# Optimization experiments

Hardware: AMD Instinct MI355X
Metric: run time of the kernel (lower is better)

The kernel has to match this reference:

```python
import jax, jax.numpy as jnp
import numpy as np

B, L, DIM, HEADS = 4, 1024, 512, 8
HD = DIM // HEADS
HID = max(64, DIM // 2)
WIN = 32
SPARSITY = 0.3
TEMP = 1.0
PAT_TAU = 0.5


def setup_inputs() -> dict:
    key = jax.random.key(0)
    ks = jax.random.split(key, 8)
    gn = lambda k, shape, sc: jax.random.normal(k, shape, jnp.float32) * sc
    return {
        "x": jax.random.normal(ks[0], (B, L, DIM), jnp.float32),
        "mask": jnp.ones((B, L), jnp.int32),
        "Wqkv": gn(ks[1], (3 * DIM, DIM), 0.02),
        "Wproj": gn(ks[2], (DIM, DIM), 0.02),
        "bproj": jnp.zeros((DIM,), jnp.float32),
        "Wsel1": gn(ks[3], (HID, DIM), 0.05),
        "bsel1": jnp.zeros((HID,), jnp.float32),
        "Wsel2": gn(ks[4], (3, HID), 0.05),
        "bsel2": jnp.zeros((3,), jnp.float32),
        "log_pattern_tau": jnp.asarray(np.log(PAT_TAU), jnp.float32),
        "sparse_w": gn(ks[5], (HEADS,), 0.2),
        "sparse_b": jnp.zeros((HEADS,), jnp.float32),
    }


def reference(x, mask, Wqkv, Wproj, bproj, Wsel1, bsel1, Wsel2, bsel2,
              log_pattern_tau, sparse_w, sparse_b):
    Bq, Lq, D = x.shape
    scale = HD ** -0.5
    qkv = (x @ Wqkv.T).reshape(Bq, Lq, 3, HEADS, HD)
    q = jnp.transpose(qkv[:, :, 0], (0, 2, 1, 3))  # (B,H,L,hd)
    k = jnp.transpose(qkv[:, :, 1], (0, 2, 1, 3))
    v = jnp.transpose(qkv[:, :, 2], (0, 2, 1, 3))
    scores = jnp.einsum('bhid,bhjd->bhij', q, k) * scale  # (B,H,L,L)

    # pattern selector on mean-pooled features (eval: no gumbel, no dropout)
    pooled = x.mean(axis=1)
    logits = jax.nn.relu(pooled @ Wsel1.T + bsel1) @ Wsel2.T + bsel2  # (B,3)
    tau = jnp.clip(jnp.exp(log_pattern_tau), 1e-4, 10.0)
    pw = jax.nn.softmax(logits / tau, axis=-1)  # (B,3)

    half = WIN // 2
    ii = jnp.arange(Lq)[:, None]
    jj = jnp.arange(Lq)[None, :]
    local = ((jj >= ii - half) & (jj <= ii + half)).astype(jnp.float32)

    # learned sparse top-k mask per head via kth-value threshold
    kk = max(1, int(Lq * (1.0 - SPARSITY)))
    s = scores * sparse_w[None, :, None, None] + sparse_b[None, :, None, None]
    kth = jax.lax.top_k(s, kk)[0][..., -1:]
    smask = (s >= kth).astype(jnp.float32)  # (B,H,L,L)

    combined = (pw[:, 0, None, None, None] * local[None, None]
                + pw[:, 1, None, None, None]
                + pw[:, 2, None, None, None] * smask)
    neg = jnp.float32(-1e9)
    scores = jnp.where(combined > 0.05, scores, neg)
    scores = jnp.where(mask[:, None, None, :] == 0, neg, scores)

    # fallback: if a row is fully masked, unmask position 0
    all_masked = jnp.all(scores <= neg + 1e-6, axis=-1)  # (B,H,L)
    scores = scores.at[..., 0].set(jnp.where(all_masked, 0.0, scores[..., 0]))

    attn = jax.nn.softmax(scores / TEMP, axis=-1)
    out = jnp.einsum('bhij,bhjd->bhid', attn, v)
    out = jnp.transpose(out, (0, 2, 1, 3)).reshape(Bq, Lq, D)
    return out @ Wproj.T + bproj
```

## Files before the change

kernel.cpp:

```cpp
#include <hip/hip_runtime.h>
#include <math.h>

typedef __attribute__((ext_vector_type(8))) short short8;
typedef __attribute__((ext_vector_type(4))) float floatx4;

#define MFMA16(a, b, c) __builtin_amdgcn_mfma_f32_16x16x32_bf16(a, b, c, 0, 0, 0)


#define FRAG512(row, k) (((size_t)((row) >> 4)) * 8192 + (((k) >> 5) * 512) + \
                         ((((k) >> 3) & 3) * 128) + (((row) & 15) * 8) + ((k) & 7))
#define FRAGQK(row, e)  (((size_t)((row) >> 4)) * 1024 + (((e) >> 5) * 512) + \
                         ((((e) >> 3) & 3) * 128) + (((row) & 15) * 8) + ((e) & 7))
#define FRAGV(key, e)   (((size_t)((key) >> 7)) * 8192 + \
                         ((((e) >> 4) * 4 + (((key) & 127) >> 5)) * 512) + \
                         (((((key) & 31) >> 3) * 16 + ((e) & 15)) * 8) + ((key) & 7))

#define OFF_XB    ((size_t)0)
#define OFF_WQKV  ((size_t)4194304)
#define OFF_WPROJ ((size_t)5767168)
#define OFF_Q     ((size_t)6291456)
#define OFF_K     ((size_t)10485760)
#define OFF_VT    ((size_t)14680064)
#define OFF_AT    ((size_t)18874368)
#define OFF_PW    ((size_t)23068672)
#define OFF_PAR   ((size_t)23069696)

__device__ __forceinline__ unsigned short f2bf(float f) {
    unsigned u = __float_as_uint(f);
    return (unsigned short)((u + 0x7fffu + ((u >> 16) & 1u)) >> 16);
}
__device__ __forceinline__ float bf2f(unsigned short s) {
    return __uint_as_float((unsigned)s << 16);
}
__device__ __forceinline__ void gl16(const void* g, void* l) {
    __builtin_amdgcn_global_load_lds(
        (const __attribute__((address_space(1))) unsigned*)g,
        (__attribute__((address_space(3))) unsigned*)l, 16, 0, 0);
}

__device__ __forceinline__ void frag_cvt_tile(const float* __restrict__ src,
                                              unsigned short* __restrict__ dst,
                                              const int t, const float sc)
{
    const int ln = t & 15, quad = (t >> 4) & 3, kh = t >> 6;
    #pragma unroll
    for (int i = 0; i < 4; ++i) {
        const int kb = kh + i * 4;
        const float* s = src + (size_t)ln * 512 + kb * 32 + quad * 8;
        float4 f0 = *(const float4*)s;
        float4 f1 = *(const float4*)(s + 4);
        unsigned short o[8] = { f2bf(f0.x * sc), f2bf(f0.y * sc), f2bf(f0.z * sc), f2bf(f0.w * sc),
                                f2bf(f1.x * sc), f2bf(f1.y * sc), f2bf(f1.z * sc), f2bf(f1.w * sc) };
        unsigned short* d = dst + kb * 512 + (size_t)(t & 63) * 8;
        *(ushort4*)d       = make_ushort4(o[0], o[1], o[2], o[3]);
        *(ushort4*)(d + 4) = make_ushort4(o[4], o[5], o[6], o[7]);
    }
}

__global__ __launch_bounds__(256)
void cvt_all(const float* __restrict__ x, const float* __restrict__ wqkv,
             const float* __restrict__ wproj, unsigned short* __restrict__ xb,
             unsigned short* __restrict__ oq, unsigned short* __restrict__ op,
             float* __restrict__ partial)
{
    const int bid = blockIdx.x, t = threadIdx.x;
    if (bid < 256) {
        const int b = bid >> 6, lb = bid & 63;
        const size_t base = ((size_t)b * 1024 + lb * 16) * 512;
        float s0 = 0.f, s1 = 0.f;
        #pragma unroll 4
        for (int l = 0; l < 16; ++l) {
            s0 += x[base + (size_t)l * 512 + t];
            s1 += x[base + (size_t)l * 512 + t + 256];
        }
        partial[((size_t)b * 64 + lb) * 512 + t] = s0;
        partial[((size_t)b * 64 + lb) * 512 + t + 256] = s1;
    } else if (bid < 512) {
        const int rt = bid - 256;
        frag_cvt_tile(x + (size_t)rt * 16 * 512, xb + (size_t)rt * 8192, t, 1.f);
    } else {
        const int tile = bid - 512;
        if (tile < 96)
            frag_cvt_tile(wqkv + (size_t)tile * 16 * 512, oq + (size_t)tile * 8192, t, 1.f);
        else
            frag_cvt_tile(wproj + (size_t)(tile - 96) * 16 * 512,
                          op + (size_t)(tile - 96) * 8192, t, 1.f);
    }
}

__global__ __launch_bounds__(256)
void selector_kernel(const float* __restrict__ partial,
                     const float* __restrict__ W1, const float* __restrict__ b1,
                     const float* __restrict__ W2, const float* __restrict__ b2,
                     const float* __restrict__ ltau, float* __restrict__ pwout)
{
    __shared__ float pooled[512];
    __shared__ float h1[256];
    __shared__ float lg[3];
    const int b = blockIdx.x, t = threadIdx.x;
    float s0 = 0.f, s1 = 0.f;
    for (int p = 0; p < 64; ++p) {
        s0 += partial[((size_t)b * 64 + p) * 512 + t];
        s1 += partial[((size_t)b * 64 + p) * 512 + t + 256];
    }
    pooled[t]       = s0 * (1.f / 1024.f);
    pooled[t + 256] = s1 * (1.f / 1024.f);
    __syncthreads();
    float acc = b1[t];
    const float* w1 = W1 + (size_t)t * 512;
    for (int d = 0; d < 512; d += 4) {
        float4 w4 = *(const float4*)(w1 + d);
        acc += w4.x * pooled[d] + w4.y * pooled[d + 1] + w4.z * pooled[d + 2] + w4.w * pooled[d + 3];
    }
    h1[t] = fmaxf(acc, 0.f);
    __syncthreads();
    if (t < 3) {
        float a = b2[t];
        const float* w2 = W2 + t * 256;
        for (int i = 0; i < 256; ++i) a += w2[i] * h1[i];
        float tauv = fminf(fmaxf(expf(ltau[0]), 1e-4f), 10.f);
        lg[t] = a / tauv;
    }
    __syncthreads();
    if (t == 0) {
        float m = fmaxf(lg[0], fmaxf(lg[1], lg[2]));
        float e0 = expf(lg[0] - m), e1 = expf(lg[1] - m), e2 = expf(lg[2] - m);
        float inv = 1.f / (e0 + e1 + e2);
        pwout[b * 3 + 0] = e0 * inv;
        pwout[b * 3 + 1] = e1 * inv;
        pwout[b * 3 + 2] = e2 * inv;
    }
}

__global__ __launch_bounds__(256)
void gemm_qkv(const unsigned short* __restrict__ xb, const unsigned short* __restrict__ wb,
              unsigned short* __restrict__ qo, unsigned short* __restrict__ ko,
              unsigned short* __restrict__ vo)
{
    __shared__ __align__(16) char smem[36864];
    unsigned short* As = (unsigned short*)smem;
    unsigned short* Bs = (unsigned short*)(smem + 8192);

    const int t = threadIdx.x;
    const int w = t >> 6, l64 = t & 63;
    const int ln = l64 & 15, quad = l64 >> 4;
    const int bx = blockIdx.x, by = blockIdx.y;
    const int m0 = by << 7, n0 = bx << 7;
    const int mw = (w & 1) << 6, nw = (w >> 1) << 6;

    floatx4 acc[4][4];
    #pragma unroll
    for (int i = 0; i < 4; ++i)
        #pragma unroll
        for (int j = 0; j < 4; ++j) acc[i][j] = (floatx4){0.f, 0.f, 0.f, 0.f};

    for (int s = 0; s < 16; ++s) {
        const int kb = s;
        #pragma unroll
        for (int ii = 0; ii < 2; ++ii) {
            const int bi = w * 2 + ii;
            gl16(xb + ((size_t)((m0 >> 4) + bi)) * 8192 + kb * 512 + l64 * 8,
                 (char*)As + bi * 1024);
            gl16(wb + ((size_t)((n0 >> 4) + bi)) * 8192 + kb * 512 + l64 * 8,
                 (char*)Bs + bi * 1024);
        }
        __syncthreads();
        short8 af[4], bf[4];
        #pragma unroll
        for (int i = 0; i < 4; ++i)
            af[i] = *(const short8*)((const char*)As + ((mw >> 4) + i) * 1024 + l64 * 16);
        #pragma unroll
        for (int j = 0; j < 4; ++j)
            bf[j] = *(const short8*)((const char*)Bs + ((nw >> 4) + j) * 1024 + l64 * 16);
        #pragma unroll
        for (int i = 0; i < 4; ++i)
            #pragma unroll
            for (int j = 0; j < 4; ++j)
                acc[i][j] = MFMA16(af[i], bf[j], acc[i][j]);
        __syncthreads();
    }

    unsigned short* tw = (unsigned short*)(smem + w * 9216);
    const int which = bx >> 2;
    const int hh = ((n0 + nw) >> 6) & 7;
    const int g = (by >> 3) * 8 + hh;
    const int lrow0 = (m0 & 1023) + mw;

    if (which == 2) {
        #pragma unroll
        for (int j = 0; j < 4; ++j)
            #pragma unroll
            for (int i = 0; i < 4; ++i)
                #pragma unroll
                for (int reg = 0; reg < 4; ++reg)
                    tw[(j * 16 + ln) * 72 + i * 16 + quad * 4 + reg] = f2bf(acc[i][j][reg]);
        const int chunk = lrow0 >> 7;
        const int ks0 = (lrow0 & 127) >> 5;
        unsigned short* dst = vo + (size_t)g * 65536 + (size_t)chunk * 8192;
        #pragma unroll
        for (int et = 0; et < 4; ++et)
            #pragma unroll
            for (int ksl = 0; ksl < 2; ++ksl) {
                const unsigned short* srcp = &tw[(et * 16 + ln) * 72 + ksl * 32 + quad * 8];
                *(short8*)(dst + (et * 4 + ks0 + ksl) * 512 + l64 * 8) = *(const short8*)srcp;
            }
    } else {
        const float sc = (which == 0) ? 0.125f : 1.f;
        #pragma unroll
        for (int j = 0; j < 4; ++j)
            #pragma unroll
            for (int i = 0; i < 4; ++i)
                #pragma unroll
                for (int reg = 0; reg < 4; ++reg)
                    tw[(i * 16 + quad * 4 + reg) * 72 + j * 16 + ln] = f2bf(acc[i][j][reg] * sc);
        unsigned short* dst = (which == 0 ? qo : ko) + (size_t)g * 65536;
        #pragma unroll
        for (int rt = 0; rt < 4; ++rt)
            #pragma unroll
            for (int eh = 0; eh < 2; ++eh) {
                const unsigned short* srcp = &tw[(rt * 16 + ln) * 72 + eh * 32 + quad * 8];
                *(short8*)(dst + ((size_t)((lrow0 >> 4) + rt)) * 1024 + eh * 512 + l64 * 8) =
                    *(const short8*)srcp;
            }
    }
}

__global__ __launch_bounds__(256)
void gemm_proj(const unsigned short* __restrict__ ab, const unsigned short* __restrict__ wb,
               const float* __restrict__ bias, float* __restrict__ out)
{
    __shared__ __align__(16) unsigned short As[8 * 512];
    __shared__ __align__(16) unsigned short Bs[4 * 512];
    const int t = threadIdx.x;
    const int w = t >> 6, l64 = t & 63;
    const int ln = l64 & 15, quad = l64 >> 4;
    const int n0 = blockIdx.x << 6;
    const int m0 = blockIdx.y << 7;
    const int mw = (w & 1) << 6, nw = (w >> 1) << 5;

    floatx4 acc[4][2];
    #pragma unroll
    for (int i = 0; i < 4; ++i)
        #pragma unroll
        for (int j = 0; j < 2; ++j) acc[i][j] = (floatx4){0.f, 0.f, 0.f, 0.f};

    for (int s = 0; s < 16; ++s) {
        #pragma unroll
        for (int ii = 0; ii < 2; ++ii) {
            const int bi = w * 2 + ii;
            gl16(ab + ((size_t)((m0 >> 4) + bi)) * 8192 + s * 512 + l64 * 8,
                 (char*)As + bi * 1024);
        }
        gl16(wb + ((size_t)((n0 >> 4) + w)) * 8192 + s * 512 + l64 * 8,
             (char*)Bs + w * 1024);
        __syncthreads();
        short8 af[4], bf[2];
        #pragma unroll
        for (int i = 0; i < 4; ++i)
            af[i] = *(const short8*)((const char*)As + ((mw >> 4) + i) * 1024 + l64 * 16);
        #pragma unroll
        for (int j = 0; j < 2; ++j)
            bf[j] = *(const short8*)((const char*)Bs + ((nw >> 4) + j) * 1024 + l64 * 16);
        #pragma unroll
        for (int i = 0; i < 4; ++i)
            #pragma unroll
            for (int j = 0; j < 2; ++j)
                acc[i][j] = MFMA16(af[i], bf[j], acc[i][j]);
        __syncthreads();
    }
    #pragma unroll
    for (int j = 0; j < 2; ++j) {
        const float bv = bias[n0 + nw + j * 16 + ln];
        #pragma unroll
        for (int i = 0; i < 4; ++i)
            #pragma unroll
            for (int reg = 0; reg < 4; ++reg)
                out[(size_t)(m0 + mw + i * 16 + quad * 4 + reg) * 512 + n0 + nw + j * 16 + ln] =
                    acc[i][j][reg] + bv;
    }
}

__global__ __launch_bounds__(256)
void attn_mfma(const unsigned short* __restrict__ qm, const unsigned short* __restrict__ km,
               const unsigned short* __restrict__ vm, const int* __restrict__ mask,
               const float* __restrict__ pw, const float* __restrict__ sw,
               const float* __restrict__ sb, unsigned short* __restrict__ aout)
{
    __shared__ int mk[1024];
    __shared__ float PO[4][16][68];
    __shared__ float msh[4][16], lsh[4][16];
    __shared__ unsigned kths[4][16];

    const int t = threadIdx.x;
    const int w = t >> 6, l64 = t & 63;
    const int ln = l64 & 15, quad = l64 >> 4;
    const int g = blockIdx.x & 31;
    const int rt = blockIdx.x >> 5;
    const int b = g >> 3, h = g & 7;
    const int i0 = rt * 16;

    const unsigned short* qg = qm + (size_t)g * 65536;
    const unsigned short* kg = km + (size_t)g * 65536;
    const unsigned short* vg = vm + (size_t)g * 65536;

    *(int4*)&mk[t * 4] = *(const int4*)(mask + b * 1024 + t * 4);

    const float pw0 = pw[b * 3 + 0], pw1 = pw[b * 3 + 1], pw2 = pw[b * 3 + 2];
    const bool a00 = pw1 > 0.05f;
    const bool a10 = (pw0 * 1.0f + pw1) > 0.05f;
    const bool a01 = (pw1 + pw2) > 0.05f;
    const bool a11 = ((pw0 * 1.0f + pw1) + pw2) > 0.05f;
    const bool need_sparse = (!a00 && a01) || (!a10 && a11);
    const bool flat_ok = (!need_sparse) && a00 && a10;
    const float w_h = sw[h], b_h = sb[h];
    __syncthreads();

    unsigned kth_r[4] = {0u, 0u, 0u, 0u};
    if (need_sparse) {
        unsigned* ub = (unsigned*)&PO[w][0][0];
        for (int r = 0; r < 16; ++r) {
            for (int c = 0; c < 16; ++c) {
                const int col = c * 64 + l64;
                float s = 0.f;
                for (int e = 0; e < 64; ++e)
                    s += bf2f(qg[FRAGQK(i0 + r, e)]) * bf2f(kg[FRAGQK(col, e)]);
                unsigned uu = __float_as_uint(s * w_h + b_h);
                ub[col] = (uu & 0x80000000u) ? ~uu : (uu | 0x80000000u);
            }
            unsigned u[16];
            #pragma unroll
            for (int c = 0; c < 16; ++c) u[c] = ub[l64 + c * 64];
            unsigned act = 0xFFFFu, p = 0u;
            int kk = 716;
            for (int bit = 31; bit >= 0; --bit) {
                unsigned ones = 0u;
                #pragma unroll
                for (int c = 0; c < 16; ++c)
                    if (((act >> c) & 1u) && ((u[c] >> bit) & 1u)) ones |= (1u << c);
                int c1 = __popc(ones);
                for (int off = 32; off; off >>= 1) c1 += __shfl_xor(c1, off);
                if (kk <= c1) { p |= (1u << bit); act &= ones; }
                else          { kk -= c1; act &= ~ones; }
            }
            if (l64 == 0) kths[w][r] = p;
        }
        #pragma unroll
        for (int reg = 0; reg < 4; ++reg) kth_r[reg] = kths[w][quad * 4 + reg];
    }

    const short8 aq0 = *(const short8*)(qg + ((size_t)(i0 >> 4)) * 1024 + l64 * 8);
    const short8 aq1 = *(const short8*)(qg + ((size_t)(i0 >> 4)) * 1024 + 512 + l64 * 8);

    float m_r[4] = {-3e38f, -3e38f, -3e38f, -3e38f};
    float l_r[4] = {0.f, 0.f, 0.f, 0.f};
    floatx4 accv[4];
    #pragma unroll
    for (int et = 0; et < 4; ++et) accv[et] = (floatx4){0.f, 0.f, 0.f, 0.f};
    unsigned short* Pw = (unsigned short*)&PO[w][0][0];

    #pragma unroll
    for (int cc = 0; cc < 2; ++cc) {
        const int j0 = (w * 2 + cc) << 7;
        const bool mall = __all((mk[j0 + l64] != 0) && (mk[j0 + 64 + l64] != 0));
        const bool fast = flat_ok && mall;

        const unsigned short* kbase = kg + ((size_t)(j0 >> 4)) * 1024 + l64 * 8;
        short8 kb0[8], kb1[8];
        #pragma unroll
        for (int nt = 0; nt < 8; ++nt) {
            kb0[nt] = *(const short8*)(kbase + nt * 1024);
            kb1[nt] = *(const short8*)(kbase + nt * 1024 + 512);
        }
        const unsigned short* vbase = vg + ((size_t)(j0 >> 7)) * 8192 + l64 * 8;
        short8 vb_cur[4], vb_nxt[4];
        #pragma unroll
        for (int ks = 0; ks < 4; ++ks)
            vb_cur[ks] = *(const short8*)(vbase + ks * 512);

        floatx4 sfr[8];
        #pragma unroll
        for (int nt = 0; nt < 8; ++nt) {
            floatx4 z = (floatx4){0.f, 0.f, 0.f, 0.f};
            z = MFMA16(aq0, kb0[nt], z);
            z = MFMA16(aq1, kb1[nt], z);
            sfr[nt] = z;
        }

        float rm[4] = {-3e38f, -3e38f, -3e38f, -3e38f};
        if (fast) {
            #pragma unroll
            for (int nt = 0; nt < 8; ++nt)
                #pragma unroll
                for (int reg = 0; reg < 4; ++reg) rm[reg] = fmaxf(rm[reg], sfr[nt][reg]);
        } else {
            #pragma unroll
            for (int nt = 0; nt < 8; ++nt) {
                const int j = j0 + nt * 16 + ln;
                const bool mk0 = (mk[j] == 0);
                #pragma unroll
                for (int reg = 0; reg < 4; ++reg) {
                    const int i = i0 + quad * 4 + reg;
                    const float s = sfr[nt][reg];
                    const bool loc = (j >= i - 16) && (j <= i + 16);
                    bool sm = false;
                    if (need_sparse) {
                        unsigned uu = __float_as_uint(s * w_h + b_h);
                        unsigned key = (uu & 0x80000000u) ? ~uu : (uu | 0x80000000u);
                        sm = key >= kth_r[reg];
                    }
                    bool allowed = loc ? (sm ? a11 : a10) : (sm ? a01 : a00);
                    if (mk0) allowed = false;
                    const float se = allowed ? s : -1e9f;
                    sfr[nt][reg] = se;
                    rm[reg] = fmaxf(rm[reg], se);
                }
            }
        }
        #pragma unroll
        for (int reg = 0; reg < 4; ++reg) {
            float v = rm[reg];
            v = fmaxf(v, __shfl_xor(v, 1));
            v = fmaxf(v, __shfl_xor(v, 2));
            v = fmaxf(v, __shfl_xor(v, 4));
            v = fmaxf(v, __shfl_xor(v, 8));
            rm[reg] = v;
        }
        float alpha[4], rs[4];
        #pragma unroll
        for (int reg = 0; reg < 4; ++reg) {
            const float mn = fmaxf(m_r[reg], rm[reg]);
            alpha[reg] = __expf(m_r[reg] - mn);
            m_r[reg] = mn;
            rs[reg] = 0.f;
        }
        #pragma unroll
        for (int nt = 0; nt < 8; ++nt)
            #pragma unroll
            for (int reg = 0; reg < 4; ++reg) {
                const float p = __expf(sfr[nt][reg] - m_r[reg]);
                rs[reg] += p;
                Pw[(quad * 4 + reg) * 136 + nt * 16 + ln] = f2bf(p);
            }
        #pragma unroll
        for (int reg = 0; reg < 4; ++reg) {
            float v = rs[reg];
            v += __shfl_xor(v, 1);
            v += __shfl_xor(v, 2);
            v += __shfl_xor(v, 4);
            v += __shfl_xor(v, 8);
            l_r[reg] = l_r[reg] * alpha[reg] + v;
        }
        short8 pa[4];
        #pragma unroll
        for (int ks = 0; ks < 4; ++ks)
            pa[ks] = *(const short8*)&Pw[ln * 136 + ks * 32 + quad * 8];
        #pragma unroll
        for (int et = 0; et < 4; ++et) {
            if (et < 3) {
                #pragma unroll
                for (int ks = 0; ks < 4; ++ks)
                    vb_nxt[ks] = *(const short8*)(vbase + ((et + 1) * 4 + ks) * 512);
            }
            floatx4 a = accv[et];
            a[0] *= alpha[0]; a[1] *= alpha[1]; a[2] *= alpha[2]; a[3] *= alpha[3];
            #pragma unroll
            for (int ks = 0; ks < 4; ++ks) a = MFMA16(pa[ks], vb_cur[ks], a);
            accv[et] = a;
            #pragma unroll
            for (int ks = 0; ks < 4; ++ks) vb_cur[ks] = vb_nxt[ks];
        }
    }

    #pragma unroll
    for (int et = 0; et < 4; ++et)
        #pragma unroll
        for (int reg = 0; reg < 4; ++reg)
            PO[w][quad * 4 + reg][et * 16 + ln] = accv[et][reg];
    if (ln == 0) {
        #pragma unroll
        for (int reg = 0; reg < 4; ++reg) {
            msh[w][quad * 4 + reg] = m_r[reg];
            lsh[w][quad * 4 + reg] = l_r[reg];
        }
    }
    __syncthreads();

    {
        const int r = t >> 4, cb = (t & 15) * 4;
        float M = fmaxf(fmaxf(msh[0][r], msh[1][r]), fmaxf(msh[2][r], msh[3][r]));
        float L = 0.f;
        float4 o = make_float4(0.f, 0.f, 0.f, 0.f);
        #pragma unroll
        for (int wv = 0; wv < 4; ++wv) {
            const float sc = __expf(msh[wv][r] - M);
            L += lsh[wv][r] * sc;
            float4 ov = *(const float4*)&PO[wv][r][cb];
            o.x += ov.x * sc; o.y += ov.y * sc; o.z += ov.z * sc; o.w += ov.w * sc;
        }
        ushort4 res;
        if (M <= -1e9f + 1e-6f) {
            res.x = vg[((cb + 0) >> 4) * 2048 + ((cb + 0) & 15) * 8];
            res.y = vg[((cb + 1) >> 4) * 2048 + ((cb + 1) & 15) * 8];
            res.z = vg[((cb + 2) >> 4) * 2048 + ((cb + 2) & 15) * 8];
            res.w = vg[((cb + 3) >> 4) * 2048 + ((cb + 3) & 15) * 8];
        } else {
            const float inv = 1.f / L;
            res.x = f2bf(o.x * inv); res.y = f2bf(o.y * inv);
            res.z = f2bf(o.z * inv); res.w = f2bf(o.w * inv);
        }
        const int row_g = b * 1024 + i0 + r;
        const int col = h * 64 + cb;
        *(ushort4*)&aout[FRAG512(row_g, col)] = res;
    }
}

extern "C" void kernel_launch(void* const* d_in, const int* in_sizes, int n_in,
                              void* d_out, int out_size, void* d_ws, size_t ws_size,
                              hipStream_t stream) {
    const float* x     = (const float*)d_in[0];
    const int*   mask  = (const int*)d_in[1];
    const float* Wqkv  = (const float*)d_in[2];
    const float* Wproj = (const float*)d_in[3];
    const float* bproj = (const float*)d_in[4];
    const float* Wsel1 = (const float*)d_in[5];
    const float* bsel1 = (const float*)d_in[6];
    const float* Wsel2 = (const float*)d_in[7];
    const float* bsel2 = (const float*)d_in[8];
    const float* ltau  = (const float*)d_in[9];
    const float* sw    = (const float*)d_in[10];
    const float* sb    = (const float*)d_in[11];
    char* ws = (char*)d_ws;
    unsigned short* xb     = (unsigned short*)(ws + OFF_XB);
    unsigned short* wqkvb  = (unsigned short*)(ws + OFF_WQKV);
    unsigned short* wprojb = (unsigned short*)(ws + OFF_WPROJ);
    unsigned short* q      = (unsigned short*)(ws + OFF_Q);
    unsigned short* k      = (unsigned short*)(ws + OFF_K);
    unsigned short* v      = (unsigned short*)(ws + OFF_VT);
    unsigned short* attnb  = (unsigned short*)(ws + OFF_AT);
    float* pw  = (float*)(ws + OFF_PW);
    float* par = (float*)(ws + OFF_PAR);
    float* out = (float*)d_out;
    (void)in_sizes; (void)n_in; (void)out_size; (void)ws_size;

    cvt_all<<<640, 256, 0, stream>>>(x, Wqkv, Wproj, xb, wqkvb, wprojb, par);
    selector_kernel<<<4, 256, 0, stream>>>(par, Wsel1, bsel1, Wsel2, bsel2, ltau, pw);
    gemm_qkv<<<dim3(12, 32), 256, 0, stream>>>(xb, wqkvb, q, k, v);
    attn_mfma<<<2048, 256, 0, stream>>>(q, k, v, mask, pw, sw, sb, attnb);
    gemm_proj<<<dim3(8, 32), 256, 0, stream>>>(attnb, wprojb, bproj, out);
}
```

Before: 163.8 us.

## Fuse selector into QKV GEMM and load MFMA fragments directly to registers

```diff
diff --git a/kernel.cpp b/kernel.cpp
--- a/kernel.cpp
+++ b/kernel.cpp
@@ -11,9 +11,6 @@
                          ((((k) >> 3) & 3) * 128) + (((row) & 15) * 8) + ((k) & 7))
 #define FRAGQK(row, e)  (((size_t)((row) >> 4)) * 1024 + (((e) >> 5) * 512) + \
                          ((((e) >> 3) & 3) * 128) + (((row) & 15) * 8) + ((e) & 7))
-#define FRAGV(key, e)   (((size_t)((key) >> 7)) * 8192 + \
-                         ((((e) >> 4) * 4 + (((key) & 127) >> 5)) * 512) + \
-                         (((((key) & 31) >> 3) * 16 + ((e) & 15)) * 8) + ((key) & 7))
 
 #define OFF_XB    ((size_t)0)
 #define OFF_WQKV  ((size_t)4194304)
@@ -31,11 +28,6 @@
 }
 __device__ __forceinline__ float bf2f(unsigned short s) {
     return __uint_as_float((unsigned)s << 16);
-}
-__device__ __forceinline__ void gl16(const void* g, void* l) {
-    __builtin_amdgcn_global_load_lds(
-        (const __attribute__((address_space(1))) unsigned*)g,
-        (__attribute__((address_space(3))) unsigned*)l, 16, 0, 0);
 }
 
 __device__ __forceinline__ void frag_cvt_tile(const float* __restrict__ src,
@@ -88,65 +80,70 @@
     }
 }
 
-__global__ __launch_bounds__(256)
-void selector_kernel(const float* __restrict__ partial,
-                     const float* __restrict__ W1, const float* __restrict__ b1,
-                     const float* __restrict__ W2, const float* __restrict__ b2,
-                     const float* __restrict__ ltau, float* __restrict__ pwout)
+__global__ __launch_bounds__(128)
+void gemm_qkv_sel(const unsigned short* __restrict__ xb, const unsigned short* __restrict__ wb,
+                  unsigned short* __restrict__ qo, unsigned short* __restrict__ ko,
+                  unsigned short* __restrict__ vo,
+                  const float* __restrict__ partial, const float* __restrict__ W1,
+                  const float* __restrict__ b1, const float* __restrict__ W2,
+                  const float* __restrict__ b2, const float* __restrict__ ltau,
+                  float* __restrict__ pwout)
 {
-    __shared__ float pooled[512];
-    __shared__ float h1[256];
-    __shared__ float lg[3];
-    const int b = blockIdx.x, t = threadIdx.x;
-    float s0 = 0.f, s1 = 0.f;
-    for (int p = 0; p < 64; ++p) {
-        s0 += partial[((size_t)b * 64 + p) * 512 + t];
-        s1 += partial[((size_t)b * 64 + p) * 512 + t + 256];
-    }
-    pooled[t]       = s0 * (1.f / 1024.f);
-    pooled[t + 256] = s1 * (1.f / 1024.f);
-    __syncthreads();
-    float acc = b1[t];
-    const float* w1 = W1 + (size_t)t * 512;
-    for (int d = 0; d < 512; d += 4) {
-        float4 w4 = *(const float4*)(w1 + d);
-        acc += w4.x * pooled[d] + w4.y * pooled[d + 1] + w4.z * pooled[d + 2] + w4.w * pooled[d + 3];
-    }
-    h1[t] = fmaxf(acc, 0.f);
-    __syncthreads();
-    if (t < 3) {
-        float a = b2[t];
-        const float* w2 = W2 + t * 256;
-        for (int i = 0; i < 256; ++i) a += w2[i] * h1[i];
-        float tauv = fminf(fmaxf(expf(ltau[0]), 1e-4f), 10.f);
-        lg[t] = a / tauv;
-    }
-    __syncthreads();
-    if (t == 0) {
-        float m = fmaxf(lg[0], fmaxf(lg[1], lg[2]));
-        float e0 = expf(lg[0] - m), e1 = expf(lg[1] - m), e2 = expf(lg[2] - m);
-        float inv = 1.f / (e0 + e1 + e2);
-        pwout[b * 3 + 0] = e0 * inv;
-        pwout[b * 3 + 1] = e1 * inv;
-        pwout[b * 3 + 2] = e2 * inv;
-    }
-}
-
-__global__ __launch_bounds__(256)
-void gemm_qkv(const unsigned short* __restrict__ xb, const unsigned short* __restrict__ wb,
-              unsigned short* __restrict__ qo, unsigned short* __restrict__ ko,
-              unsigned short* __restrict__ vo)
-{
-    __shared__ __align__(16) char smem[36864];
-    unsigned short* As = (unsigned short*)smem;
-    unsigned short* Bs = (unsigned short*)(smem + 8192);
-
+    __shared__ __align__(16) unsigned short tile[2][64 * 72];
+    const int bx = blockIdx.x, by = blockIdx.y;
     const int t = threadIdx.x;
+
+    if (by == 64) {
+        if (bx >= 4) return;
+        float* pooled = (float*)&tile[0][0];
+        float* h1 = pooled + 512;
+        float* lg = h1 + 256;
+        const int b = bx;
+        #pragma unroll
+        for (int c = 0; c < 4; ++c) {
+            const int col = t + c * 128;
+            float s = 0.f;
+            for (int p = 0; p < 64; ++p) s += partial[((size_t)b * 64 + p) * 512 + col];
+            pooled[col] = s * (1.f / 1024.f);
+        }
+        __syncthreads();
+        for (int r = t; r < 256; r += 128) {
+            float acc = b1[r];
+            const float* w1 = W1 + (size_t)r * 512;
+            for (int d = 0; d < 512; d += 4) {
+                float4 w4 = *(const float4*)(w1 + d);
+                acc += w4.x * pooled[d] + w4.y * pooled[d + 1] +
+                       w4.z * pooled[d + 2] + w4.w * pooled[d + 3];
+            }
+            h1[r] = fmaxf(acc, 0.f);
+        }
+        __syncthreads();
+        if (t < 3) {
+            float a = b2[t];
+            const float* w2 = W2 + t * 256;
+            for (int i = 0; i < 256; ++i) a += w2[i] * h1[i];
+            float tauv = fminf(fmaxf(expf(ltau[0]), 1e-4f), 10.f);
+            lg[t] = a / tauv;
+        }
+        __syncthreads();
+        if (t == 0) {
+            float m = fmaxf(lg[0], fmaxf(lg[1], lg[2]));
+            float e0 = expf(lg[0] - m), e1 = expf(lg[1] - m), e2 = expf(lg[2] - m);
+            float inv = 1.f / (e0 + e1 + e2);
+            pwout[b * 3 + 0] = e0 * inv;
+            pwout[b * 3 + 1] = e1 * inv;
+            pwout[b * 3 + 2] = e2 * inv;
+        }
+        return;
+    }
+
     const int w = t >> 6, l64 = t & 63;
     const int ln = l64 & 15, quad = l64 >> 4;
-    const int bx = blockIdx.x, by = blockIdx.y;
-    const int m0 = by << 7, n0 = bx << 7;
-    const int mw = (w & 1) << 6, nw = (w >> 1) << 6;
+    const int m0 = by << 6;
+    const int nb0 = (bx << 7) + (w << 6);
+
+    const unsigned short* Abase = xb + ((size_t)(m0 >> 4)) * 8192 + l64 * 8;
+    const unsigned short* Bbase = wb + ((size_t)(nb0 >> 4)) * 8192 + l64 * 8;
 
     floatx4 acc[4][4];
     #pragma unroll
@@ -154,37 +151,43 @@
         #pragma unroll
         for (int j = 0; j < 4; ++j) acc[i][j] = (floatx4){0.f, 0.f, 0.f, 0.f};
 
-    for (int s = 0; s < 16; ++s) {
-        const int kb = s;
-        #pragma unroll
-        for (int ii = 0; ii < 2; ++ii) {
-            const int bi = w * 2 + ii;
-            gl16(xb + ((size_t)((m0 >> 4) + bi)) * 8192 + kb * 512 + l64 * 8,
-                 (char*)As + bi * 1024);
-            gl16(wb + ((size_t)((n0 >> 4) + bi)) * 8192 + kb * 512 + l64 * 8,
-                 (char*)Bs + bi * 1024);
-        }
-        __syncthreads();
-        short8 af[4], bf[4];
+    short8 a0[4], b0[4], a1[4], b1v[4];
+    #pragma unroll
+    for (int i = 0; i < 4; ++i) {
+        a0[i] = *(const short8*)(Abase + (size_t)i * 8192);
+        b0[i] = *(const short8*)(Bbase + (size_t)i * 8192);
+    }
+    for (int s = 0; s < 16; s += 2) {
+        #pragma unroll
+        for (int i = 0; i < 4; ++i) {
+            a1v: ;
+            a1[i]  = *(const short8*)(Abase + (size_t)i * 8192 + (s + 1) * 512);
+            b1v[i] = *(const short8*)(Bbase + (size_t)i * 8192 + (s + 1) * 512);
+        }
         #pragma unroll
         for (int i = 0; i < 4; ++i)
-            af[i] = *(const short8*)((const char*)As + ((mw >> 4) + i) * 1024 + l64 * 16);
-        #pragma unroll
-        for (int j = 0; j < 4; ++j)
-            bf[j] = *(const short8*)((const char*)Bs + ((nw >> 4) + j) * 1024 + l64 * 16);
+            #pragma unroll
+            for (int j = 0; j < 4; ++j)
+                acc[i][j] = MFMA16(a0[i], b0[j], acc[i][j]);
+        if (s + 2 < 16) {
+            #pragma unroll
+            for (int i = 0; i < 4; ++i) {
+                a0[i] = *(const short8*)(Abase + (size_t)i * 8192 + (s + 2) * 512);
+                b0[i] = *(const short8*)(Bbase + (size_t)i * 8192 + (s + 2) * 512);
+            }
+        }
         #pragma unroll
         for (int i = 0; i < 4; ++i)
             #pragma unroll
             for (int j = 0; j < 4; ++j)
-                acc[i][j] = MFMA16(af[i], bf[j], acc[i][j]);
-        __syncthreads();
-    }
-
-    unsigned short* tw = (unsigned short*)(smem + w * 9216);
+                acc[i][j] = MFMA16(a1[i], b1v[j], acc[i][j]);
+    }
+
+    unsigned short* tw = &tile[w][0];
     const int which = bx >> 2;
-    const int hh = ((n0 + nw) >> 6) & 7;
-    const int g = (by >> 3) * 8 + hh;
-    const int lrow0 = (m0 & 1023) + mw;
+    const int hh = (nb0 >> 6) & 7;
+    const int g = (by >> 4) * 8 + hh;
+    const int lrow0 = m0 & 1023;
 
     if (which == 2) {
         #pragma unroll
@@ -225,57 +228,61 @@
     }
 }
 
-__global__ __launch_bounds__(256)
+__global__ __launch_bounds__(64)
 void gemm_proj(const unsigned short* __restrict__ ab, const unsigned short* __restrict__ wb,
                const float* __restrict__ bias, float* __restrict__ out)
 {
-    __shared__ __align__(16) unsigned short As[8 * 512];
-    __shared__ __align__(16) unsigned short Bs[4 * 512];
     const int t = threadIdx.x;
-    const int w = t >> 6, l64 = t & 63;
-    const int ln = l64 & 15, quad = l64 >> 4;
-    const int n0 = blockIdx.x << 6;
-    const int m0 = blockIdx.y << 7;
-    const int mw = (w & 1) << 6, nw = (w >> 1) << 5;
-
-    floatx4 acc[4][2];
+    const int ln = t & 15, quad = t >> 4;
+    const int n0 = blockIdx.x << 6, m0 = blockIdx.y << 6;
+
+    const unsigned short* Abase = ab + ((size_t)(m0 >> 4)) * 8192 + t * 8;
+    const unsigned short* Bbase = wb + ((size_t)(n0 >> 4)) * 8192 + t * 8;
+
+    floatx4 acc[4][4];
     #pragma unroll
     for (int i = 0; i < 4; ++i)
         #pragma unroll
-        for (int j = 0; j < 2; ++j) acc[i][j] = (floatx4){0.f, 0.f, 0.f, 0.f};
-
-    for (int s = 0; s < 16; ++s) {
-        #pragma unroll
-        for (int ii = 0; ii < 2; ++ii) {
-            const int bi = w * 2 + ii;
-            gl16(ab + ((size_t)((m0 >> 4) + bi)) * 8192 + s * 512 + l64 * 8,
-                 (char*)As + bi * 1024);
-        }
-        gl16(wb + ((size_t)((n0 >> 4) + w)) * 8192 + s * 512 + l64 * 8,
-             (char*)Bs + w * 1024);
-        __syncthreads();
-        short8 af[4], bf[2];
+        for (int j = 0; j < 4; ++j) acc[i][j] = (floatx4){0.f, 0.f, 0.f, 0.f};
+
+    short8 a0[4], b0[4], a1[4], b1v[4];
+    #pragma unroll
+    for (int i = 0; i < 4; ++i) {
+        a0[i] = *(const short8*)(Abase + (size_t)i * 8192);
+        b0[i] = *(const short8*)(Bbase + (size_t)i * 8192);
+    }
+    for (int s = 0; s < 16; s += 2) {
+        #pragma unroll
+        for (int i = 0; i < 4; ++i) {
+            a1[i]  = *(const short8*)(Abase + (size_t)i * 8192 + (s + 1) * 512);
+            b1v[i] = *(const short8*)(Bbase + (size_t)i * 8192 + (s + 1) * 512);
+        }
         #pragma unroll
         for (int i = 0; i < 4; ++i)
-            af[i] = *(const short8*)((const char*)As + ((mw >> 4) + i) * 1024 + l64 * 16);
-        #pragma unroll
-        for (int j = 0; j < 2; ++j)
-            bf[j] = *(const short8*)((const char*)Bs + ((nw >> 4) + j) * 1024 + l64 * 16);
+            #pragma unroll
+            for (int j = 0; j < 4; ++j)
+                acc[i][j] = MFMA16(a0[i], b0[j], acc[i][j]);
+        if (s + 2 < 16) {
+            #pragma unroll
+            for (int i = 0; i < 4; ++i) {
+                a0[i] = *(const short8*)(Abase + (size_t)i * 8192 + (s + 2) * 512);
+                b0[i] = *(const short8*)(Bbase + (size_t)i * 8192 + (s + 2) * 512);
+            }
+        }
         #pragma unroll
         for (int i = 0; i < 4; ++i)
             #pragma unroll
-            for (int j = 0; j < 2; ++j)
-                acc[i][j] = MFMA16(af[i], bf[j], acc[i][j]);
-        __syncthreads();
-    }
-    #pragma unroll
-    for (int j = 0; j < 2; ++j) {
-        const float bv = bias[n0 + nw + j * 16 + ln];
+            for (int j = 0; j < 4; ++j)
+                acc[i][j] = MFMA16(a1[i], b1v[j], acc[i][j]);
+    }
+    #pragma unroll
+    for (int j = 0; j < 4; ++j) {
+        const float bv = bias[n0 + j * 16 + ln];
         #pragma unroll
         for (int i = 0; i < 4; ++i)
             #pragma unroll
             for (int reg = 0; reg < 4; ++reg)
-                out[(size_t)(m0 + mw + i * 16 + quad * 4 + reg) * 512 + n0 + nw + j * 16 + ln] =
+                out[(size_t)(m0 + i * 16 + quad * 4 + reg) * 512 + n0 + j * 16 + ln] =
                     acc[i][j][reg] + bv;
     }
 }
@@ -543,8 +550,8 @@
     (void)in_sizes; (void)n_in; (void)out_size; (void)ws_size;
 
     cvt_all<<<640, 256, 0, stream>>>(x, Wqkv, Wproj, xb, wqkvb, wprojb, par);
-    selector_kernel<<<4, 256, 0, stream>>>(par, Wsel1, bsel1, Wsel2, bsel2, ltau, pw);
-    gemm_qkv<<<dim3(12, 32), 256, 0, stream>>>(xb, wqkvb, q, k, v);
+    gemm_qkv_sel<<<dim3(12, 65), 128, 0, stream>>>(xb, wqkvb, q, k, v,
+                                                   par, Wsel1, bsel1, Wsel2, bsel2, ltau, pw);
     attn_mfma<<<2048, 256, 0, stream>>>(q, k, v, mask, pw, sw, sb, attnb);
-    gemm_proj<<<dim3(8, 32), 256, 0, stream>>>(attnb, wprojb, bproj, out);
-}
+    gemm_proj<<<dim3(8, 64), 64, 0, stream>>>(attnb, wprojb, bproj, out);
+}
```

Measured after the change: 158.9 us. 3.0% less time.
